# Optimization experiments

Hardware: AMD Instinct MI355X
Metric: run time of the kernel (lower is better)

Reference implementation:

```python
import jax, jax.numpy as jnp
import numpy as np

NUM_HEADS = 16
ROPE_THETA = 1000.0


def _rope(x, cos, sin):
    # x: [B, H, T, d_k]; cos/sin: [T, d_k//2]
    xp = x.reshape(x.shape[:-1] + (x.shape[-1] // 2, 2))
    xe, xo = xp[..., 0], xp[..., 1]
    c = cos[None, None, :, :]
    s = sin[None, None, :, :]
    re = xe * c - xo * s
    ro = xe * s + xo * c
    return jnp.stack((re, ro), axis=-1).reshape(x.shape)


def setup_inputs() -> dict:
    key = jax.random.key(0)
    ks = jax.random.split(key, 5)
    B, T, D = 2, 2048, 1024
    std = 2.0 / (D + D)
    return {
        "x": jax.random.normal(ks[0], (B, T, D), dtype=jnp.float32),
        "wq": jax.random.normal(ks[1], (D, D), dtype=jnp.float32) * std,
        "wk": jax.random.normal(ks[2], (D, D), dtype=jnp.float32) * std,
        "wv": jax.random.normal(ks[3], (D, D), dtype=jnp.float32) * std,
        "wo": jax.random.normal(ks[4], (D, D), dtype=jnp.float32) * std,
    }


def reference(x, wq, wk, wv, wo):
    B, T, D = x.shape
    H = NUM_HEADS
    dk = D // H

    def proj(w):
        # Linear stores weight as [out, in]: '... in, out in -> ... out'
        y = jnp.einsum('btd,ed->bte', x, w)
        return y.reshape(B, T, H, dk).transpose(0, 2, 1, 3)  # [B,H,T,dk]

    q = proj(wq)
    k = proj(wk)
    v = proj(wv)

    # RoPE tables
    pos = jnp.arange(T, dtype=jnp.float32)[:, None]
    kidx = jnp.arange(dk // 2, dtype=jnp.float32)
    inv_freq = ROPE_THETA ** (-2.0 * kidx / dk)
    ang = pos * inv_freq[None, :]
    cos, sin = jnp.cos(ang), jnp.sin(ang)

    q = _rope(q, cos, sin)
    k = _rope(k, cos, sin)

    scores = jnp.einsum('bhnd,bhmd->bhnm', q, k) / jnp.sqrt(jnp.asarray(dk, x.dtype))
    causal = jnp.tril(jnp.ones((T, T), dtype=bool))
    scores = jnp.where(causal[None, None], scores, -jnp.inf)
    attn = jax.nn.softmax(scores, axis=-1)
    head = jnp.einsum('bhnm,bhmd->bhnd', attn, v)  # [B,H,T,dk]

    concat = head.transpose(0, 2, 1, 3).reshape(B, T, D)
    return jnp.einsum('btd,ed->bte', concat, wo)
```

## Files before the change

### kernel.cpp

```cpp
#include <hip/hip_runtime.h>
#include <hip/hip_bf16.h>

typedef __hip_bfloat16 bf16;
typedef __attribute__((ext_vector_type(8))) short bf16x8;
typedef __attribute__((ext_vector_type(4))) float f32x4;

#define T_SEQ 2048
#define NHEADS 16
#define DK 64
#define DMODEL 1024

__device__ inline void load_lds16(const void* g, void* l) {
    __builtin_amdgcn_global_load_lds((const __attribute__((address_space(1))) void*)g,
                                     (__attribute__((address_space(3))) void*)l, 16, 0, 0);
}

__global__ void cvt_all(const float* __restrict__ x,  const float* __restrict__ wq,
                        const float* __restrict__ wk, const float* __restrict__ wv,
                        const float* __restrict__ wo, bf16* __restrict__ xb,
                        bf16* __restrict__ wqkvb, bf16* __restrict__ wob,
                        float4* __restrict__ zacc) {
    int i = blockIdx.x * blockDim.x + threadIdx.x;
    if (i >= (1 << 21)) {
        zacc[i - (1 << 21)] = make_float4(0.f, 0.f, 0.f, 0.f);
        return;
    }
    const float* src; bf16* dst; int off;
    if (i < (1 << 20)) { src = x; dst = xb; off = i; }
    else {
        int j = i - (1 << 20);
        int seg = j >> 18; off = j & ((1 << 18) - 1);
        src = (seg == 0) ? wq : (seg == 1) ? wk : (seg == 2) ? wv : wo;
        dst = (seg < 3) ? (wqkvb + ((size_t)seg << 20)) : wob;
    }
    float4 f = ((const float4*)src)[off];
    ushort4 o;
    o.x = __bfloat16_as_ushort(__float2bfloat16(f.x));
    o.y = __bfloat16_as_ushort(__float2bfloat16(f.y));
    o.z = __bfloat16_as_ushort(__float2bfloat16(f.z));
    o.w = __bfloat16_as_ushort(__float2bfloat16(f.w));
    ((ushort4*)dst)[off] = o;
}

__global__ __launch_bounds__(256, 4) void gemm_qkv_rope(const bf16* __restrict__ A,
                                                        const bf16* __restrict__ B,
                                                        bf16* __restrict__ qb,
                                                        bf16* __restrict__ kb,
                                                        bf16* __restrict__ vt) {
    const int K = 1024;
    __shared__ bf16 As[128 * 64];
    __shared__ bf16 Bs[128 * 64];
    const int tid  = threadIdx.x;
    const int lane = tid & 63;
    const int wave = tid >> 6;
    const int l16  = lane & 15;
    const int quad = lane >> 4;
    const int wy = wave >> 1, wx = wave & 1;
    const int brow = blockIdx.y * 128;
    const int bcol = blockIdx.x * 128;
    const int sw0 = (quad ^ (l16 & 7)) * 8;
    const int sw1 = ((4 + quad) ^ (l16 & 7)) * 8;

    f32x4 acc[4][4] = {};

    for (int k0 = 0; k0 < K; k0 += 64) {
#pragma unroll
        for (int i = 0; i < 4; ++i) {
            int j   = tid + 256 * i;
            int row = j >> 3;
            int blk = (j & 7) ^ (row & 7);
            load_lds16(A + (size_t)(brow + row) * K + k0 + blk * 8, (char*)As + j * 16);
            load_lds16(B + (size_t)(bcol + row) * K + k0 + blk * 8, (char*)Bs + j * 16);
        }
        __syncthreads();
#pragma unroll
        for (int ks = 0; ks < 2; ++ks) {
            const int sw = ks ? sw1 : sw0;
            bf16x8 af[4], bq[4];
#pragma unroll
            for (int i = 0; i < 4; ++i)
                af[i] = *(const bf16x8*)(As + (wy * 64 + i * 16 + l16) * 64 + sw);
#pragma unroll
            for (int j = 0; j < 4; ++j)
                bq[j] = *(const bf16x8*)(Bs + (wx * 64 + j * 16 + l16) * 64 + sw);
#pragma unroll
            for (int i = 0; i < 4; ++i)
#pragma unroll
                for (int j = 0; j < 4; ++j)
                    acc[i][j] = __builtin_amdgcn_mfma_f32_16x16x32_bf16(bq[j], af[i], acc[i][j], 0, 0, 0);
        }
        __syncthreads();
    }
    const int seg = bcol >> 10;
    const int hh  = ((bcol & 1023) >> 6) + wx;
    if (seg < 2) {
        bf16* dst = seg ? kb : qb;
        const float osc = seg ? 1.0f : 0.18033688011112042f;
#pragma unroll
        for (int i = 0; i < 4; ++i) {
            int trow = brow + wy * 64 + i * 16 + l16;
            int t = trow & (T_SEQ - 1), bi = trow >> 11;
            float tf = (float)t;
            bf16* base = dst + ((size_t)(bi * NHEADS + hh) * T_SEQ + t) * DK;
#pragma unroll
            for (int j = 0; j < 4; ++j) {
                ushort4 u;
#pragma unroll
                for (int p = 0; p < 2; ++p) {
                    const float inv = exp2f(-0.31143075889f * (float)(j * 8 + quad * 2 + p));
                    float s, c;
                    __sincosf(tf * inv, &s, &c);
                    float xe = acc[i][j][2 * p], xo = acc[i][j][2 * p + 1];
                    float re = fmaf(-xo, s, xe * c) * osc;
                    float ro = fmaf(xe, s, xo * c) * osc;
                    ((unsigned short*)&u)[2 * p] =
                        __bfloat16_as_ushort(__float2bfloat16(re));
                    ((unsigned short*)&u)[2 * p + 1] =
                        __bfloat16_as_ushort(__float2bfloat16(ro));
                }
                *(ushort4*)(base + j * 16 + quad * 4) = u;
            }
        }
    } else {
#pragma unroll
        for (int j = 0; j < 4; ++j)
#pragma unroll
            for (int i = 0; i < 4; ++i)
#pragma unroll
                for (int r = 0; r < 4; ++r) {
                    int d    = j * 16 + quad * 4 + r;
                    int tcol = brow + wy * 64 + i * 16 + l16;
                    int t = tcol & (T_SEQ - 1), bi = tcol >> 11;
                    vt[((size_t)(bi * NHEADS + hh) * DK + d) * T_SEQ + t] =
                        __float2bfloat16(acc[i][j][r]);
                }
    }
}

__global__ __launch_bounds__(256, 4) void gemm_bt(const bf16* __restrict__ A,
                                                  const bf16* __restrict__ B,
                                                  float* __restrict__ C,
                                                  int M, int N, int K) {
    __shared__ bf16 As[128 * 64];
    __shared__ bf16 Bs[128 * 64];
    const int tid  = threadIdx.x;
    const int lane = tid & 63;
    const int wave = tid >> 6;
    const int l16  = lane & 15;
    const int quad = lane >> 4;
    const int wy = wave >> 1, wx = wave & 1;
    const int brow = blockIdx.y * 128;
    const int bcol = blockIdx.x * 128;
    const int sw0 = (quad ^ (l16 & 7)) * 8;
    const int sw1 = ((4 + quad) ^ (l16 & 7)) * 8;

    f32x4 acc[4][4] = {};

    for (int k0 = 0; k0 < K; k0 += 64) {
#pragma unroll
        for (int i = 0; i < 4; ++i) {
            int j   = tid + 256 * i;
            int row = j >> 3;
            int blk = (j & 7) ^ (row & 7);
            load_lds16(A + (size_t)(brow + row) * K + k0 + blk * 8, (char*)As + j * 16);
            load_lds16(B + (size_t)(bcol + row) * K + k0 + blk * 8, (char*)Bs + j * 16);
        }
        __syncthreads();
#pragma unroll
        for (int ks = 0; ks < 2; ++ks) {
            const int sw = ks ? sw1 : sw0;
            bf16x8 af[4], bq[4];
#pragma unroll
            for (int i = 0; i < 4; ++i)
                af[i] = *(const bf16x8*)(As + (wy * 64 + i * 16 + l16) * 64 + sw);
#pragma unroll
            for (int j = 0; j < 4; ++j)
                bq[j] = *(const bf16x8*)(Bs + (wx * 64 + j * 16 + l16) * 64 + sw);
#pragma unroll
            for (int i = 0; i < 4; ++i)
#pragma unroll
                for (int j = 0; j < 4; ++j)
                    acc[i][j] = __builtin_amdgcn_mfma_f32_16x16x32_bf16(af[i], bq[j], acc[i][j], 0, 0, 0);
        }
        __syncthreads();
    }
#pragma unroll
    for (int i = 0; i < 4; ++i)
#pragma unroll
        for (int j = 0; j < 4; ++j)
#pragma unroll
            for (int r = 0; r < 4; ++r) {
                int row = brow + wy * 64 + i * 16 + quad * 4 + r;
                int col = bcol + wx * 64 + j * 16 + l16;
                C[(size_t)row * N + col] = acc[i][j][r];
            }
}

__constant__ unsigned char c_sched[24] = {
    28, 61, 57, 58, 24, 53, 49, 20,
    62, 54, 50, 41, 42, 16, 45, 46,
     0,  4,  8, 12, 33, 37, 34, 38};

__global__ __launch_bounds__(256, 4) void attn_kernel(const bf16* __restrict__ qb,
                                                      const bf16* __restrict__ kb,
                                                      const bf16* __restrict__ vt,
                                                      float* __restrict__ Oacc,
                                                      float* __restrict__ Lacc,
                                                      bf16* __restrict__ conc) {
    __shared__ bf16 Ks[2][64 * 64];
    __shared__ bf16 Vs[2][64 * 64];
    __shared__ bf16 Pl[4][16 * 64];
    const int bh = blockIdx.y;
    const int b = bh >> 4, h = bh & 15;

    const int e    = c_sched[blockIdx.x];
    const int tile = e >> 2, mode = e & 3;
    const int it0  = (mode == 2) ? tile + 1 : 0;
    const int it1  = (mode == 1) ? tile : 2 * tile + 1;
    const bool partial = (mode != 0);
    const int qbase = tile << 7;

    const int tid = threadIdx.x;
    const int lane = tid & 63, wave = tid >> 6;
    const int l16 = lane & 15, quad = lane >> 4;
    const int qr0 = qbase + wave * 16;
    const int qr1 = qr0 + 64;

    const bf16* Qp = qb + (size_t)bh * T_SEQ * DK;
    const bf16* Kp = kb + (size_t)bh * T_SEQ * DK;
    const bf16* Vp = vt + (size_t)bh * DK * T_SEQ;
    char* Pw = (char*)&Pl[wave][0];

    const short one_bits = 0x3F80;
    const bf16x8 ones = {one_bits, one_bits, one_bits, one_bits,
                         one_bits, one_bits, one_bits, one_bits};

    bf16x8 qf[2][2];
#pragma unroll
    for (int s = 0; s < 2; ++s) {
        qf[0][s] = *(const bf16x8*)(Qp + (size_t)(qr0 + l16) * DK + s * 32 + quad * 8);
        qf[1][s] = *(const bf16x8*)(Qp + (size_t)(qr1 + l16) * DK + s * 32 + quad * 8);
    }

    auto stage = [&](int bb, int k0) {
        int j = tid;
#pragma unroll
        for (int i = 0; i < 2; ++i, j += 256) {
            int row = j >> 3, cbl = (j & 7) ^ ((j >> 3) & 7);
            load_lds16(Kp + (size_t)(k0 + row) * DK + cbl * 8, (char*)Ks[bb] + j * 16);
        }
        j = tid;
#pragma unroll
        for (int i = 0; i < 2; ++i, j += 256) {
            int row = j >> 3, cbl = (j & 7) ^ ((j >> 3) & 7);
            load_lds16(Vp + (size_t)row * T_SEQ + k0 + cbl * 8, (char*)Vs[bb] + j * 16);
        }
    };

    f32x4 o0[4] = {}, o1[4] = {};
    f32x4 ol0 = {}, ol1 = {};
    const int sw0 = (quad ^ (l16 & 7)) * 8;
    const int sw1 = ((4 + quad) ^ (l16 & 7)) * 8;
    const int pw_wr_base = l16 * 128 + (quad & 1) * 8;
    const int pq = quad >> 1;

    int cur = 0;
    stage(0, it0 * 64);
    if (it0 < it1) stage(1, (it0 + 1) * 64);
    for (int it = it0; it <= it1; ++it) {
        if (it < it1) asm volatile("s_waitcnt vmcnt(4)" ::: "memory");
        else          asm volatile("s_waitcnt vmcnt(0)" ::: "memory");
        __builtin_amdgcn_s_barrier();
        __builtin_amdgcn_sched_barrier(0);

        const int k0 = it * 64;
        const bool skip0 = (k0 > qr0 + 15);
        const bool diag0 = (k0 + 63 > qr0) && !skip0;
        const bool diag1 = (k0 + 63 > qr1);

        f32x4 s0[4] = {}, s1[4] = {};
        __builtin_amdgcn_s_setprio(1);
#pragma unroll
        for (int nt = 0; nt < 4; ++nt) {
            bf16x8 kf0 = *(const bf16x8*)(Ks[cur] + (nt * 16 + l16) * 64 + sw0);
            bf16x8 kf1 = *(const bf16x8*)(Ks[cur] + (nt * 16 + l16) * 64 + sw1);
            if (!skip0) {
                s0[nt] = __builtin_amdgcn_mfma_f32_16x16x32_bf16(kf0, qf[0][0], s0[nt], 0, 0, 0);
                s0[nt] = __builtin_amdgcn_mfma_f32_16x16x32_bf16(kf1, qf[0][1], s0[nt], 0, 0, 0);
            }
            s1[nt] = __builtin_amdgcn_mfma_f32_16x16x32_bf16(kf0, qf[1][0], s1[nt], 0, 0, 0);
            s1[nt] = __builtin_amdgcn_mfma_f32_16x16x32_bf16(kf1, qf[1][1], s1[nt], 0, 0, 0);
        }
        __builtin_amdgcn_s_setprio(0);

        if (!skip0) {
#pragma unroll
            for (int nt = 0; nt < 4; ++nt) {
                union { bf16 hv[4]; uint2 u; } pk;
#pragma unroll
                for (int r = 0; r < 4; ++r) {
                    float v = s0[nt][r];
                    if (diag0 && (k0 + nt * 16 + quad * 4 + r > qr0 + l16)) v = -30.0f;
                    pk.hv[r] = __float2bfloat16(exp2f(v));
                }
                *(uint2*)(Pw + pw_wr_base + (((nt * 2 + pq) ^ (l16 & 7)) << 4)) = pk.u;
            }
            __builtin_amdgcn_s_setprio(1);
#pragma unroll
            for (int ks = 0; ks < 2; ++ks) {
                bf16x8 pf = *(const bf16x8*)(Pw + l16 * 128 + (((ks * 4 + quad) ^ (l16 & 7)) << 4));
                const int sw = ks ? sw1 : sw0;
                ol0 = __builtin_amdgcn_mfma_f32_16x16x32_bf16(pf, ones, ol0, 0, 0, 0);
#pragma unroll
                for (int j = 0; j < 4; ++j) {
                    bf16x8 vf = *(const bf16x8*)(Vs[cur] + (j * 16 + l16) * 64 + sw);
                    o0[j] = __builtin_amdgcn_mfma_f32_16x16x32_bf16(pf, vf, o0[j], 0, 0, 0);
                }
            }
            __builtin_amdgcn_s_setprio(0);
        }

#pragma unroll
        for (int nt = 0; nt < 4; ++nt) {
            union { bf16 hv[4]; uint2 u; } pk;
#pragma unroll
            for (int r = 0; r < 4; ++r) {
                float v = s1[nt][r];
                if (diag1 && (k0 + nt * 16 + quad * 4 + r > qr1 + l16)) v = -30.0f;
                pk.hv[r] = __float2bfloat16(exp2f(v));
            }
            *(uint2*)(Pw + pw_wr_base + (((nt * 2 + pq) ^ (l16 & 7)) << 4)) = pk.u;
        }
        __builtin_amdgcn_s_setprio(1);
#pragma unroll
        for (int ks = 0; ks < 2; ++ks) {
            bf16x8 pf = *(const bf16x8*)(Pw + l16 * 128 + (((ks * 4 + quad) ^ (l16 & 7)) << 4));
            const int sw = ks ? sw1 : sw0;
            ol1 = __builtin_amdgcn_mfma_f32_16x16x32_bf16(pf, ones, ol1, 0, 0, 0);
#pragma unroll
            for (int j = 0; j < 4; ++j) {
                bf16x8 vf = *(const bf16x8*)(Vs[cur] + (j * 16 + l16) * 64 + sw);
                o1[j] = __builtin_amdgcn_mfma_f32_16x16x32_bf16(pf, vf, o1[j], 0, 0, 0);
            }
        }
        __builtin_amdgcn_s_setprio(0);

        __builtin_amdgcn_sched_barrier(0);
        __builtin_amdgcn_s_barrier();
        if (it + 2 <= it1) stage(cur, (it + 2) * 64);
        cur ^= 1;
    }

#pragma unroll
    for (int g = 0; g < 2; ++g) {
        const f32x4* op = g ? o1 : o0;
        const f32x4 lv = g ? ol1 : ol0;
        const int qr = g ? qr1 : qr0;
        if (!partial) {
#pragma unroll
            for (int r = 0; r < 4; ++r) {
                float inv_l = 1.0f / lv[r];
                int t = qr + quad * 4 + r;
#pragma unroll
                for (int j = 0; j < 4; ++j)
                    conc[((size_t)b * T_SEQ + t) * DMODEL + h * DK + j * 16 + l16] =
                        __float2bfloat16(op[j][r] * inv_l);
            }
        } else {
#pragma unroll
            for (int r = 0; r < 4; ++r) {
                int q = qr + quad * 4 + r;
                if (l16 == 0)
                    atomicAdd(&Lacc[(size_t)bh * 1024 + q - 1024], lv[r]);
                float* Ob = Oacc + ((size_t)bh * 1024 + q - 1024) * DK;
#pragma unroll
                for (int j = 0; j < 4; ++j)
                    atomicAdd(&Ob[j * 16 + l16], op[j][r]);
            }
        }
    }
}

__global__ void attn_finalize(const float* __restrict__ Oacc, const float* __restrict__ Lacc,
                              bf16* __restrict__ conc) {
    int i4 = blockIdx.x * blockDim.x + threadIdx.x;
    if (i4 >= (1 << 19)) return;
    int bhq = i4 >> 4;
    int d4  = i4 & 15;
    int bh = bhq >> 10, q1 = bhq & 1023;
    int b = bh >> 4, h = bh & 15;
    int q = 1024 + q1;
    float inv = 1.0f / Lacc[bhq];
    float4 o4 = ((const float4*)Oacc)[i4];
    ushort4 u;
    u.x = __bfloat16_as_ushort(__float2bfloat16(o4.x * inv));
    u.y = __bfloat16_as_ushort(__float2bfloat16(o4.y * inv));
    u.z = __bfloat16_as_ushort(__float2bfloat16(o4.z * inv));
    u.w = __bfloat16_as_ushort(__float2bfloat16(o4.w * inv));
    *(ushort4*)&conc[((size_t)(b * T_SEQ + q)) * DMODEL + h * DK + d4 * 4] = u;
}

extern "C" void kernel_launch(void* const* d_in, const int* in_sizes, int n_in,
                              void* d_out, int out_size, void* d_ws, size_t ws_size,
                              hipStream_t stream) {
    const float* x  = (const float*)d_in[0];
    const float* wq = (const float*)d_in[1];
    const float* wk = (const float*)d_in[2];
    const float* wv = (const float*)d_in[3];
    const float* wo = (const float*)d_in[4];
    float* out = (float*)d_out;

    char* ws = (char*)d_ws;
    bf16* xb    = (bf16*)(ws);
    bf16* wqkvb = (bf16*)(ws + (8ull << 20));
    bf16* wob   = (bf16*)(ws + (14ull << 20));
    bf16* conc  = (bf16*)(ws + (16ull << 20));
    float* Oacc = (float*)(ws + (24ull << 20));
    float* Lacc = (float*)(ws + (32ull << 20));
    bf16* qb    = (bf16*)(ws + (40ull << 20));
    bf16* kb    = (bf16*)(ws + (48ull << 20));
    bf16* vt    = (bf16*)(ws + (56ull << 20));

    cvt_all<<<10272, 256, 0, stream>>>(x, wq, wk, wv, wo, xb, wqkvb, wob,
                                       (float4*)Oacc);
    gemm_qkv_rope<<<dim3(24, 32), 256, 0, stream>>>(xb, wqkvb, qb, kb, vt);

    attn_kernel<<<dim3(24, 32), 256, 0, stream>>>(qb, kb, vt, Oacc, Lacc, conc);
    attn_finalize<<<2048, 256, 0, stream>>>(Oacc, Lacc, conc);

    gemm_bt<<<dim3(8, 32), 256, 0, stream>>>(conc, wob, out, 4096, 1024, 1024);
}
```

Measured before the change: 179.5 us.

## Switch attention to 32x32x16 MFMA tiles with register-shuffled P operand

Measured after the change: 181.6 us. No clear change (+1.1%).

```diff
diff --git a/kernel.cpp b/kernel.cpp
--- a/kernel.cpp
+++ b/kernel.cpp
@@ -4,6 +4,7 @@
 typedef __hip_bfloat16 bf16;
 typedef __attribute__((ext_vector_type(8))) short bf16x8;
 typedef __attribute__((ext_vector_type(4))) float f32x4;
+typedef __attribute__((ext_vector_type(16))) float f32x16;
 
 #define T_SEQ 2048
 #define NHEADS 16
@@ -13,6 +14,12 @@
 __device__ inline void load_lds16(const void* g, void* l) {
     __builtin_amdgcn_global_load_lds((const __attribute__((address_space(1))) void*)g,
                                      (__attribute__((address_space(3))) void*)l, 16, 0, 0);
+}
+
+__device__ inline unsigned pk_bf16(float lo, float hi) {
+    unsigned a = __bfloat16_as_ushort(__float2bfloat16(lo));
+    unsigned b = __bfloat16_as_ushort(__float2bfloat16(hi));
+    return a | (b << 16);
 }
 
 __global__ void cvt_all(const float* __restrict__ x,  const float* __restrict__ wq,
@@ -201,7 +208,7 @@
     62, 54, 50, 41, 42, 16, 45, 46,
      0,  4,  8, 12, 33, 37, 34, 38};
 
-__global__ __launch_bounds__(256, 4) void attn_kernel(const bf16* __restrict__ qb,
+__global__ __launch_bounds__(256, 3) void attn_kernel(const bf16* __restrict__ qb,
                                                       const bf16* __restrict__ kb,
                                                       const bf16* __restrict__ vt,
                                                       float* __restrict__ Oacc,
@@ -209,7 +216,6 @@
                                                       bf16* __restrict__ conc) {
     __shared__ bf16 Ks[2][64 * 64];
     __shared__ bf16 Vs[2][64 * 64];
-    __shared__ bf16 Pl[4][16 * 64];
     const int bh = blockIdx.y;
     const int b = bh >> 4, h = bh & 15;
 
@@ -222,25 +228,21 @@
 
     const int tid = threadIdx.x;
     const int lane = tid & 63, wave = tid >> 6;
-    const int l16 = lane & 15, quad = lane >> 4;
-    const int qr0 = qbase + wave * 16;
-    const int qr1 = qr0 + 64;
+    const int l31 = lane & 31, hi = lane >> 5;
+    const int qr = qbase + wave * 32;
 
     const bf16* Qp = qb + (size_t)bh * T_SEQ * DK;
     const bf16* Kp = kb + (size_t)bh * T_SEQ * DK;
     const bf16* Vp = vt + (size_t)bh * DK * T_SEQ;
-    char* Pw = (char*)&Pl[wave][0];
 
     const short one_bits = 0x3F80;
     const bf16x8 ones = {one_bits, one_bits, one_bits, one_bits,
                          one_bits, one_bits, one_bits, one_bits};
 
-    bf16x8 qf[2][2];
-#pragma unroll
-    for (int s = 0; s < 2; ++s) {
-        qf[0][s] = *(const bf16x8*)(Qp + (size_t)(qr0 + l16) * DK + s * 32 + quad * 8);
-        qf[1][s] = *(const bf16x8*)(Qp + (size_t)(qr1 + l16) * DK + s * 32 + quad * 8);
-    }
+    bf16x8 qf[4];
+#pragma unroll
+    for (int s = 0; s < 4; ++s)
+        qf[s] = *(const bf16x8*)(Qp + (size_t)(qr + l31) * DK + s * 16 + hi * 8);
 
     auto stage = [&](int bb, int k0) {
         int j = tid;
@@ -257,12 +259,8 @@
         }
     };
 
-    f32x4 o0[4] = {}, o1[4] = {};
-    f32x4 ol0 = {}, ol1 = {};
-    const int sw0 = (quad ^ (l16 & 7)) * 8;
-    const int sw1 = ((4 + quad) ^ (l16 & 7)) * 8;
-    const int pw_wr_base = l16 * 128 + (quad & 1) * 8;
-    const int pq = quad >> 1;
+    f32x16 o0 = {}, o1 = {};
+    f32x16 ol = {};
 
     int cur = 0;
     stage(0, it0 * 64);
@@ -274,76 +272,69 @@
         __builtin_amdgcn_sched_barrier(0);
 
         const int k0 = it * 64;
-        const bool skip0 = (k0 > qr0 + 15);
-        const bool diag0 = (k0 + 63 > qr0) && !skip0;
-        const bool diag1 = (k0 + 63 > qr1);
-
-        f32x4 s0[4] = {}, s1[4] = {};
-        __builtin_amdgcn_s_setprio(1);
-#pragma unroll
-        for (int nt = 0; nt < 4; ++nt) {
-            bf16x8 kf0 = *(const bf16x8*)(Ks[cur] + (nt * 16 + l16) * 64 + sw0);
-            bf16x8 kf1 = *(const bf16x8*)(Ks[cur] + (nt * 16 + l16) * 64 + sw1);
-            if (!skip0) {
-                s0[nt] = __builtin_amdgcn_mfma_f32_16x16x32_bf16(kf0, qf[0][0], s0[nt], 0, 0, 0);
-                s0[nt] = __builtin_amdgcn_mfma_f32_16x16x32_bf16(kf1, qf[0][1], s0[nt], 0, 0, 0);
-            }
-            s1[nt] = __builtin_amdgcn_mfma_f32_16x16x32_bf16(kf0, qf[1][0], s1[nt], 0, 0, 0);
-            s1[nt] = __builtin_amdgcn_mfma_f32_16x16x32_bf16(kf1, qf[1][1], s1[nt], 0, 0, 0);
-        }
-        __builtin_amdgcn_s_setprio(0);
-
-        if (!skip0) {
-#pragma unroll
-            for (int nt = 0; nt < 4; ++nt) {
-                union { bf16 hv[4]; uint2 u; } pk;
-#pragma unroll
-                for (int r = 0; r < 4; ++r) {
-                    float v = s0[nt][r];
-                    if (diag0 && (k0 + nt * 16 + quad * 4 + r > qr0 + l16)) v = -30.0f;
-                    pk.hv[r] = __float2bfloat16(exp2f(v));
+#pragma unroll
+        for (int sub = 0; sub < 2; ++sub) {
+            const int kb0 = k0 + sub * 32;
+            if (kb0 > qr + 31) continue;
+            const int krow = sub * 32 + l31;
+
+            f32x16 sacc = {};
+            __builtin_amdgcn_s_setprio(1);
+#pragma unroll
+            for (int s = 0; s < 4; ++s) {
+                bf16x8 kf = *(const bf16x8*)((char*)Ks[cur] + krow * 128 +
+                                             (((2 * s + hi) ^ (krow & 7)) << 4));
+                sacc = __builtin_amdgcn_mfma_f32_32x32x16_bf16(kf, qf[s], sacc, 0, 0, 0);
+            }
+            __builtin_amdgcn_s_setprio(0);
+
+            const bool diagS = (kb0 + 31) > qr;
+            float p[16];
+#pragma unroll
+            for (int r = 0; r < 16; ++r) {
+                float v = sacc[r];
+                if (diagS && (kb0 + (r & 3) + 8 * (r >> 2) + 4 * hi > qr + l31))
+                    v = -30.0f;
+                p[r] = exp2f(v);
+            }
+
+            bf16x8 pa[2];
+#pragma unroll
+            for (int kh = 0; kh < 2; ++kh) {
+                unsigned a0 = pk_bf16(p[8 * kh + 0], p[8 * kh + 1]);
+                unsigned a1 = pk_bf16(p[8 * kh + 2], p[8 * kh + 3]);
+                unsigned b0 = pk_bf16(p[8 * kh + 4], p[8 * kh + 5]);
+                unsigned b1 = pk_bf16(p[8 * kh + 6], p[8 * kh + 7]);
+                unsigned t0 = hi ? a0 : b0;
+                unsigned t1 = hi ? a1 : b1;
+                unsigned x0 = (unsigned)__shfl_xor((int)t0, 32);
+                unsigned x1 = (unsigned)__shfl_xor((int)t1, 32);
+                union { unsigned u[4]; bf16x8 v; } pu;
+                pu.u[0] = hi ? x0 : a0;
+                pu.u[1] = hi ? x1 : a1;
+                pu.u[2] = hi ? b0 : x0;
+                pu.u[3] = hi ? b1 : x1;
+                pa[kh] = pu.v;
+            }
+
+            __builtin_amdgcn_s_setprio(1);
+            ol = __builtin_amdgcn_mfma_f32_32x32x16_bf16(pa[0], ones, ol, 0, 0, 0);
+            ol = __builtin_amdgcn_mfma_f32_32x32x16_bf16(pa[1], ones, ol, 0, 0, 0);
+#pragma unroll
+            for (int j = 0; j < 2; ++j) {
+                const int vrow = j * 32 + l31;
+#pragma unroll
+                for (int kh = 0; kh < 2; ++kh) {
+                    bf16x8 vf = *(const bf16x8*)((char*)Vs[cur] + vrow * 128 +
+                                 (((4 * sub + 2 * kh + hi) ^ (vrow & 7)) << 4));
+                    if (j == 0)
+                        o0 = __builtin_amdgcn_mfma_f32_32x32x16_bf16(pa[kh], vf, o0, 0, 0, 0);
+                    else
+                        o1 = __builtin_amdgcn_mfma_f32_32x32x16_bf16(pa[kh], vf, o1, 0, 0, 0);
                 }
-                *(uint2*)(Pw + pw_wr_base + (((nt * 2 + pq) ^ (l16 & 7)) << 4)) = pk.u;
-            }
-            __builtin_amdgcn_s_setprio(1);
-#pragma unroll
-            for (int ks = 0; ks < 2; ++ks) {
-                bf16x8 pf = *(const bf16x8*)(Pw + l16 * 128 + (((ks * 4 + quad) ^ (l16 & 7)) << 4));
-                const int sw = ks ? sw1 : sw0;
-                ol0 = __builtin_amdgcn_mfma_f32_16x16x32_bf16(pf, ones, ol0, 0, 0, 0);
-#pragma unroll
-                for (int j = 0; j < 4; ++j) {
-                    bf16x8 vf = *(const bf16x8*)(Vs[cur] + (j * 16 + l16) * 64 + sw);
-                    o0[j] = __builtin_amdgcn_mfma_f32_16x16x32_bf16(pf, vf, o0[j], 0, 0, 0);
-                }
             }
             __builtin_amdgcn_s_setprio(0);
         }
-
-#pragma unroll
-        for (int nt = 0; nt < 4; ++nt) {
-            union { bf16 hv[4]; uint2 u; } pk;
-#pragma unroll
-            for (int r = 0; r < 4; ++r) {
-                float v = s1[nt][r];
-                if (diag1 && (k0 + nt * 16 + quad * 4 + r > qr1 + l16)) v = -30.0f;
-                pk.hv[r] = __float2bfloat16(exp2f(v));
-            }
-            *(uint2*)(Pw + pw_wr_base + (((nt * 2 + pq) ^ (l16 & 7)) << 4)) = pk.u;
-        }
-        __builtin_amdgcn_s_setprio(1);
-#pragma unroll
-        for (int ks = 0; ks < 2; ++ks) {
-            bf16x8 pf = *(const bf16x8*)(Pw + l16 * 128 + (((ks * 4 + quad) ^ (l16 & 7)) << 4));
-            const int sw = ks ? sw1 : sw0;
-            ol1 = __builtin_amdgcn_mfma_f32_16x16x32_bf16(pf, ones, ol1, 0, 0, 0);
-#pragma unroll
-            for (int j = 0; j < 4; ++j) {
-                bf16x8 vf = *(const bf16x8*)(Vs[cur] + (j * 16 + l16) * 64 + sw);
-                o1[j] = __builtin_amdgcn_mfma_f32_16x16x32_bf16(pf, vf, o1[j], 0, 0, 0);
-            }
-        }
-        __builtin_amdgcn_s_setprio(0);
 
         __builtin_amdgcn_sched_barrier(0);
         __builtin_amdgcn_s_barrier();
@@ -352,31 +343,19 @@
     }
 
 #pragma unroll
-    for (int g = 0; g < 2; ++g) {
-        const f32x4* op = g ? o1 : o0;
-        const f32x4 lv = g ? ol1 : ol0;
-        const int qr = g ? qr1 : qr0;
+    for (int r = 0; r < 16; ++r) {
+        const int q = qr + (r & 3) + 8 * (r >> 2) + 4 * hi;
         if (!partial) {
-#pragma unroll
-            for (int r = 0; r < 4; ++r) {
-                float inv_l = 1.0f / lv[r];
-                int t = qr + quad * 4 + r;
-#pragma unroll
-                for (int j = 0; j < 4; ++j)
-                    conc[((size_t)b * T_SEQ + t) * DMODEL + h * DK + j * 16 + l16] =
-                        __float2bfloat16(op[j][r] * inv_l);
-            }
+            float inv_l = 1.0f / ol[r];
+            size_t base = ((size_t)b * T_SEQ + q) * DMODEL + h * DK;
+            conc[base + l31]      = __float2bfloat16(o0[r] * inv_l);
+            conc[base + 32 + l31] = __float2bfloat16(o1[r] * inv_l);
         } else {
-#pragma unroll
-            for (int r = 0; r < 4; ++r) {
-                int q = qr + quad * 4 + r;
-                if (l16 == 0)
-                    atomicAdd(&Lacc[(size_t)bh * 1024 + q - 1024], lv[r]);
-                float* Ob = Oacc + ((size_t)bh * 1024 + q - 1024) * DK;
-#pragma unroll
-                for (int j = 0; j < 4; ++j)
-                    atomicAdd(&Ob[j * 16 + l16], op[j][r]);
-            }
+            if (l31 == 0)
+                atomicAdd(&Lacc[(size_t)bh * 1024 + q - 1024], ol[r]);
+            float* Ob = Oacc + ((size_t)bh * 1024 + q - 1024) * DK;
+            atomicAdd(&Ob[l31], o0[r]);
+            atomicAdd(&Ob[32 + l31], o1[r]);
         }
     }
 }
```
